# Optimization experiments

Hardware: AMD Instinct MI355X
Metric: run time of the kernel (lower is better)

## Reference

```python
import jax, jax.numpy as jnp
import numpy as np
import math

D_MODEL = 1024
NHEAD = 16
D_HEAD = D_MODEL // NHEAD
TAU = 300.0
DELTA = 5.0 * 60.0  # delta_minutes -> seconds


def setup_inputs() -> dict:
    key = jax.random.key(0)
    ks = jax.random.split(key, 10)
    B, M = 4, 2048
    H = jax.random.normal(ks[0], (B, M, D_MODEL), dtype=jnp.float32)
    patch_mask = jax.random.randint(ks[1], (B, M), 0, 2).astype(jnp.int32)
    s = 1.0 / math.sqrt(D_MODEL)
    Wq = jax.random.normal(ks[2], (D_MODEL, D_MODEL), dtype=jnp.float32) * s
    bq = jnp.zeros((D_MODEL,), dtype=jnp.float32)
    Wk = jax.random.normal(ks[3], (D_MODEL, D_MODEL), dtype=jnp.float32) * s
    bk = jnp.zeros((D_MODEL,), dtype=jnp.float32)
    Wv = jax.random.normal(ks[4], (D_MODEL, D_MODEL), dtype=jnp.float32) * s
    bv = jnp.zeros((D_MODEL,), dtype=jnp.float32)
    Wo = jax.random.normal(ks[5], (D_MODEL, D_MODEL), dtype=jnp.float32) * s
    bo = jnp.zeros((D_MODEL,), dtype=jnp.float32)
    return {"H": H, "patch_mask": patch_mask, "Wq": Wq, "bq": bq,
            "Wk": Wk, "bk": bk, "Wv": Wv, "bv": bv, "Wo": Wo, "bo": bo}


def _time_bias(M):
    idx = jnp.arange(M)
    dist = jnp.abs(idx[:, None] - idx[None, :]).astype(jnp.float32) * DELTA
    w = jnp.exp(-dist / max(TAU, 1e-6))
    return jnp.log(w + 1e-12)  # (M, M)


def reference(H, patch_mask, Wq, bq, Wk, bk, Wv, bv, Wo, bo):
    B, M, D = H.shape
    nh, dh = NHEAD, D_HEAD
    # projections -> (B, nh, M, dh)
    q = (H @ Wq.T + bq).reshape(B, M, nh, dh).transpose(0, 2, 1, 3)
    k = (H @ Wk.T + bk).reshape(B, M, nh, dh).transpose(0, 2, 1, 3)
    v = (H @ Wv.T + bv).reshape(B, M, nh, dh).transpose(0, 2, 1, 3)
    attn = jnp.einsum('bhqd,bhkd->bhqk', q, k) / math.sqrt(dh)
    attn = attn + _time_bias(M)[None, None, :, :]
    key_pad = patch_mask <= 0  # (B, M)
    attn = jnp.where(key_pad[:, None, None, :], -1e9, attn)
    A = jax.nn.softmax(attn, axis=-1)
    out = jnp.einsum('bhqk,bhkd->bhqd', A, v)
    out = out.transpose(0, 2, 1, 3).reshape(B, M, D)
    out = out @ Wo.T + bo
    out = out * patch_mask[:, :, None].astype(out.dtype)
    return out
```

## Files before the change

### kernel.cpp

```cpp
#include <hip/hip_runtime.h>
#include <stdint.h>

typedef short short8 __attribute__((ext_vector_type(8)));
typedef float f32x4 __attribute__((ext_vector_type(4)));

#define B_    4
#define M_    2048
#define D_    1024
#define NH_   16
#define DH_   64
#define LOG2E 1.44269504f

__device__ __forceinline__ short f2bf(float f) {
  union { float f; uint32_t u; } v; v.f = f;
  uint32_t r = (v.u + 0x7fffu + ((v.u >> 16) & 1u)) >> 16;
  return (short)r;
}

__device__ __forceinline__ void gl_lds16(const void* g, void* l) {
  __builtin_amdgcn_global_load_lds(
      (__attribute__((address_space(1))) void*)(g),
      (__attribute__((address_space(3))) void*)(l),
      16, 0, 0);
}

__device__ __forceinline__ f32x4 mfma16(short8 a, short8 b, f32x4 c) {
  return __builtin_amdgcn_mfma_f32_16x16x32_bf16(a, b, c, 0, 0, 0);
}

__global__ __launch_bounds__(256) void cvt_all(const float* __restrict__ H,
                                               const float* __restrict__ s0,
                                               const float* __restrict__ s1,
                                               const float* __restrict__ s2,
                                               const float* __restrict__ s3,
                                               short* __restrict__ dH,
                                               short* __restrict__ d0,
                                               short* __restrict__ d1,
                                               short* __restrict__ d2,
                                               short* __restrict__ d3) {
  const int bidx = blockIdx.x;
  const float* src;
  short* dst;
  int i;
  if (bidx < 8192) {
    src = H; dst = dH; i = bidx * 256 + threadIdx.x;
  } else {
    const int y = (bidx - 8192) >> 10;
    src = (y == 0) ? s0 : (y == 1) ? s1 : (y == 2) ? s2 : s3;
    dst = (y == 0) ? d0 : (y == 1) ? d1 : (y == 2) ? d2 : d3;
    i = ((bidx - 8192) & 1023) * 256 + threadIdx.x;
  }
  float4 v = ((const float4*)src)[i];
  short4 o;
  o.x = f2bf(v.x); o.y = f2bf(v.y); o.z = f2bf(v.z); o.w = f2bf(v.w);
  ((short4*)dst)[i] = o;
}

__global__ __launch_bounds__(256, 2) void gemm_qkv(const short* __restrict__ A,
                                                   const short* __restrict__ Wqb,
                                                   const short* __restrict__ Wkb,
                                                   const short* __restrict__ Wvb,
                                                   const float* __restrict__ bq,
                                                   const float* __restrict__ bk,
                                                   const float* __restrict__ bv,
                                                   short* __restrict__ Qo,
                                                   short* __restrict__ Ko,
                                                   short* __restrict__ Vo) {
  __shared__ char smem_raw[65536];
  short* Ab0 = (short*)smem_raw;
  short* Ab1 = (short*)(smem_raw + 8192);

  const int L = blockIdx.x + 8 * blockIdx.y;
  const int xcd = L & 7;
  const int s = L >> 3;
  const int m_local = s & 7;
  const int nt = s >> 3;
  const int m0 = (xcd * 8 + m_local) * 128;
  const int n0 = nt * 128;

  const int tid = threadIdx.x;
  const int w = tid >> 6, l = tid & 63;
  const int q4 = l >> 4, c = l & 15;
  const int wr = w >> 1, wc = w & 1;

  f32x4 acc[3][4][4] = {};
  const int arow = (l >> 2);
  const int acol = ((l & 3) ^ ((l >> 3) & 3)) * 8;
  const int q4s = (q4 ^ ((c >> 1) & 3)) * 8;

  const short* Bz0 = Wqb;
  const short* Bz1 = Wkb;
  const short* Bz2 = Wvb;

#pragma unroll
  for (int st = 0; st < 2; ++st) {
    const int chunk = w * 2 + st;
    const size_t roff = (size_t)(chunk * 16 + arow) * 1024 + acol;
    gl_lds16(A + (size_t)m0 * 1024 + roff, Ab0 + chunk * 512);
    gl_lds16(Bz0 + (size_t)n0 * 1024 + roff, (short*)(smem_raw + 16384) + chunk * 512);
    gl_lds16(Bz1 + (size_t)n0 * 1024 + roff, (short*)(smem_raw + 32768) + chunk * 512);
    gl_lds16(Bz2 + (size_t)n0 * 1024 + roff, (short*)(smem_raw + 49152) + chunk * 512);
  }
  __syncthreads();

  for (int kk = 0; kk < 32; ++kk) {
    const int cur = kk & 1;
    if (kk + 1 < 32) {
      const int k0n = (kk + 1) * 32;
#pragma unroll
      for (int st = 0; st < 2; ++st) {
        const int chunk = w * 2 + st;
        const size_t roff = (size_t)(chunk * 16 + arow) * 1024 + k0n + acol;
        gl_lds16(A + (size_t)m0 * 1024 + roff, (cur ? Ab0 : Ab1) + chunk * 512);
        gl_lds16(Bz0 + (size_t)n0 * 1024 + roff,
                 (short*)(smem_raw + 16384 + (cur ? 0 : 8192)) + chunk * 512);
        gl_lds16(Bz1 + (size_t)n0 * 1024 + roff,
                 (short*)(smem_raw + 32768 + (cur ? 0 : 8192)) + chunk * 512);
        gl_lds16(Bz2 + (size_t)n0 * 1024 + roff,
                 (short*)(smem_raw + 49152 + (cur ? 0 : 8192)) + chunk * 512);
      }
    }
    const short* Ab = cur ? Ab1 : Ab0;
    short8 af[4];
#pragma unroll
    for (int i = 0; i < 4; ++i)
      af[i] = *(const short8*)(Ab + (wr * 64 + i * 16 + c) * 32 + q4s);
#pragma unroll
    for (int z = 0; z < 3; ++z) {
      const short* Bb =
          (const short*)(smem_raw + 16384 + z * 16384 + (cur ? 8192 : 0));
      short8 bfr[4];
#pragma unroll
      for (int j = 0; j < 4; ++j)
        bfr[j] = *(const short8*)(Bb + (wc * 64 + j * 16 + c) * 32 + q4s);
#pragma unroll
      for (int i = 0; i < 4; ++i)
#pragma unroll
        for (int j = 0; j < 4; ++j)
          acc[z][i][j] = mfma16(af[i], bfr[j], acc[z][i][j]);
    }
    __syncthreads();
  }

#pragma unroll
  for (int z = 0; z < 2; ++z) {
    short* Cb = (short*)smem_raw;
    const float* bias = z ? bk : bq;
    short* outp = z ? Ko : Qo;
    const float scale = z ? 1.0f : 0.125f;
#pragma unroll
    for (int j = 0; j < 4; ++j) {
      const float bvv = bias[n0 + wc * 64 + j * 16 + c];
#pragma unroll
      for (int i = 0; i < 4; ++i)
#pragma unroll
        for (int r = 0; r < 4; ++r)
          Cb[(wr * 64 + i * 16 + q4 * 4 + r) * 136 + wc * 64 + j * 16 + c] =
              f2bf((acc[z][i][j][r] + bvv) * scale);
    }
    __syncthreads();
#pragma unroll
    for (int p = 0; p < 8; ++p) {
      const int g = p * 256 + tid;
      const int row = g >> 4, seg = g & 15;
      *(short8*)(outp + (size_t)(m0 + row) * 1024 + n0 + seg * 8) =
          *(const short8*)(Cb + row * 136 + seg * 8);
    }
    __syncthreads();
  }
  {
    short* Cb = (short*)smem_raw;
#pragma unroll
    for (int j = 0; j < 4; ++j) {
      const float bvv = bv[n0 + wc * 64 + j * 16 + c];
#pragma unroll
      for (int i = 0; i < 4; ++i) {
        short4 pk;
        pk.x = f2bf(acc[2][i][j][0] + bvv);
        pk.y = f2bf(acc[2][i][j][1] + bvv);
        pk.z = f2bf(acc[2][i][j][2] + bvv);
        pk.w = f2bf(acc[2][i][j][3] + bvv);
        *(short4*)(Cb + (wc * 64 + j * 16 + c) * 136 + wr * 64 + i * 16 + q4 * 4) = pk;
      }
    }
    __syncthreads();
    const int bb = m0 >> 11;
    const int tokb = m0 & 2047;
#pragma unroll
    for (int p = 0; p < 8; ++p) {
      const int g = p * 256 + tid;
      const int col = g >> 4, rseg = g & 15;
      const int colg = n0 + col;
      const int hh = colg >> 6, dd = colg & 63;
      *(short8*)(Vo + ((size_t)(bb * NH_ + hh) * DH_ + dd) * M_ + tokb + rseg * 8) =
          *(const short8*)(Cb + col * 136 + rseg * 8);
    }
  }
}

__global__ __launch_bounds__(256) void gemm_oproj(const short* __restrict__ A,
                                                  const short* __restrict__ Bt,
                                                  const float* __restrict__ bias,
                                                  const int* __restrict__ pmask,
                                                  float* __restrict__ outp) {
  __shared__ char smem[24576];
  short* Ab0 = (short*)smem;
  short* Ab1 = (short*)(smem + 8192);
  short* Bb0 = (short*)(smem + 16384);
  short* Bb1 = (short*)(smem + 20480);

  const int L = blockIdx.x + 16 * blockIdx.y;
  const int xcd = L & 7;
  const int s = L >> 3;
  const int m_local = s & 7;
  const int nt = s >> 3;
  const int m0 = (xcd * 8 + m_local) * 128;
  const int n0 = nt * 64;

  const int tid = threadIdx.x;
  const int w = tid >> 6, l = tid & 63;
  const int q4 = l >> 4, c = l & 15;
  const int wr = w >> 1, wc = w & 1;

  f32x4 acc[4][2] = {};
  const int arow = (l >> 2);
  const int acol = (l & 3) * 8;

#pragma unroll
  for (int st = 0; st < 2; ++st) {
    const int chunk = w * 2 + st;
    gl_lds16(A + (size_t)(m0 + chunk * 16 + arow) * 1024 + acol, Ab0 + chunk * 512);
  }
  gl_lds16(Bt + (size_t)(n0 + w * 16 + arow) * 1024 + acol, Bb0 + w * 512);
  __syncthreads();

  for (int kk = 0; kk < 32; ++kk) {
    const int cur = kk & 1;
    if (kk + 1 < 32) {
      const int k0n = (kk + 1) * 32;
#pragma unroll
      for (int st = 0; st < 2; ++st) {
        const int chunk = w * 2 + st;
        gl_lds16(A + (size_t)(m0 + chunk * 16 + arow) * 1024 + k0n + acol,
                 (cur ? Ab0 : Ab1) + chunk * 512);
      }
      gl_lds16(Bt + (size_t)(n0 + w * 16 + arow) * 1024 + k0n + acol,
               (cur ? Bb0 : Bb1) + w * 512);
    }
    const short* Ab = cur ? Ab1 : Ab0;
    const short* Bb = cur ? Bb1 : Bb0;
    short8 af[4], bfr[2];
#pragma unroll
    for (int i = 0; i < 4; ++i)
      af[i] = *(const short8*)(Ab + (wr * 64 + i * 16 + c) * 32 + q4 * 8);
#pragma unroll
    for (int j = 0; j < 2; ++j)
      bfr[j] = *(const short8*)(Bb + (wc * 32 + j * 16 + c) * 32 + q4 * 8);
#pragma unroll
    for (int i = 0; i < 4; ++i)
#pragma unroll
      for (int j = 0; j < 2; ++j)
        acc[i][j] = mfma16(af[i], bfr[j], acc[i][j]);
    __syncthreads();
  }

  float* Cf = (float*)smem;
#pragma unroll
  for (int half = 0; half < 2; ++half) {
    __syncthreads();
    if (wr == half) {
#pragma unroll
      for (int j = 0; j < 2; ++j) {
        const float bvv = bias[n0 + wc * 32 + j * 16 + c];
#pragma unroll
        for (int i = 0; i < 4; ++i)
#pragma unroll
          for (int r = 0; r < 4; ++r)
            Cf[(i * 16 + q4 * 4 + r) * 68 + wc * 32 + j * 16 + c] =
                acc[i][j][r] + bvv;
      }
    }
    __syncthreads();
#pragma unroll
    for (int p = 0; p < 4; ++p) {
      const int g = p * 256 + tid;
      const int row = g >> 4, seg = g & 15;
      const int rowg = m0 + half * 64 + row;
      const float mmv = (pmask[rowg] > 0) ? 1.0f : 0.0f;
      float4 v = *(const float4*)(Cf + row * 68 + seg * 4);
      v.x *= mmv; v.y *= mmv; v.z *= mmv; v.w *= mmv;
      *(float4*)(outp + (size_t)rowg * 1024 + n0 + seg * 4) = v;
    }
  }
}

__global__ __launch_bounds__(256) void attn_kernel(const short* __restrict__ Qb,
                                                   const short* __restrict__ Kb,
                                                   const short* __restrict__ Vtb,
                                                   const int* __restrict__ pmask,
                                                   short* __restrict__ Attb) {
  __shared__ char smem[20480];
  short* Ks0 = (short*)smem;
  short* Ks1 = (short*)(smem + 4096);
  short* Vs0 = (short*)(smem + 8192);
  short* Vs1 = (short*)(smem + 12288);
  short* Ps  = (short*)(smem + 16384);

  const int tid = threadIdx.x;
  const int w = tid >> 6, l = tid & 63;
  const int q4 = l >> 4, c = l & 15;
  const int qt = blockIdx.x, h = blockIdx.y, b = blockIdx.z;
  const short* Qrow = Qb + (size_t)(b * M_) * D_ + h * DH_;
  const short* Kbase = Kb + (size_t)(b * M_) * D_ + h * DH_;
  const short* Vbase = Vtb + (size_t)(b * NH_ + h) * DH_ * M_;
  const int qrow0 = qt * 64 + w * 16;

  short8 aq0 = *(const short8*)(Qrow + (size_t)(qrow0 + c) * D_ + q4 * 8);
  short8 aq1 = *(const short8*)(Qrow + (size_t)(qrow0 + c) * D_ + 32 + q4 * 8);

  const int jt0 = max(0, 2 * qt - 2);
  const int jt1 = min(M_ / 32 - 1, 2 * qt + 3);

  const int kh = tid >> 7, krow = (tid >> 2) & 31, ch = tid & 3;
  const int vrow = tid >> 2;

  {
    const int j0 = jt0 * 32;
    gl_lds16(Kbase + (size_t)(j0 + krow) * D_ + kh * 32 + ch * 8, (char*)Ks0 + tid * 16);
    gl_lds16(Vbase + (size_t)vrow * M_ + j0 + ch * 8, (char*)Vs0 + tid * 16);
  }
  __syncthreads();

  f32x4 o[4] = {};
  float lrun[4] = {0.f, 0.f, 0.f, 0.f};
  short* Pw = Ps + w * 512;

  for (int jt = jt0; jt <= jt1; ++jt) {
    const int buf = (jt - jt0) & 1;
    const int j0 = jt * 32;
    if (jt < jt1) {
      const int j0n = j0 + 32;
      gl_lds16(Kbase + (size_t)(j0n + krow) * D_ + kh * 32 + ch * 8,
               (char*)(buf ? Ks0 : Ks1) + tid * 16);
      gl_lds16(Vbase + (size_t)vrow * M_ + j0n + ch * 8,
               (char*)(buf ? Vs0 : Vs1) + tid * 16);
    }
    const short* Kt = buf ? Ks1 : Ks0;
    const short* Vt = buf ? Vs1 : Vs0;
    short8 b00 = *(const short8*)(Kt + c * 32 + q4 * 8);
    short8 b10 = *(const short8*)(Kt + 1024 + c * 32 + q4 * 8);
    short8 b01 = *(const short8*)(Kt + (16 + c) * 32 + q4 * 8);
    short8 b11 = *(const short8*)(Kt + 1024 + (16 + c) * 32 + q4 * 8);
    f32x4 s0 = {}, s1 = {};
    s0 = mfma16(aq0, b00, s0);
    s0 = mfma16(aq1, b10, s0);
    s1 = mfma16(aq0, b01, s1);
    s1 = mfma16(aq1, b11, s1);

    const float w0m = (pmask[b * M_ + j0 + c] > 0) ? 1.f : 0.f;
    const float w1m = (pmask[b * M_ + j0 + 16 + c] > 0) ? 1.f : 0.f;

#pragma unroll
    for (int r = 0; r < 4; ++r) {
      const int qr = qrow0 + q4 * 4 + r;
      const float d0 = fminf(fabsf((float)(qr - (j0 + c))), 28.0f);
      const float d1 = fminf(fabsf((float)(qr - (j0 + 16 + c))), 28.0f);
      const float p0 = exp2f((s0[r] - d0) * LOG2E) * w0m;
      const float p1 = exp2f((s1[r] - d1) * LOG2E) * w1m;
      Pw[(q4 * 4 + r) * 32 + c] = f2bf(p0);
      Pw[(q4 * 4 + r) * 32 + 16 + c] = f2bf(p1);
      lrun[r] += p0 + p1;
    }
    short8 pa = *(const short8*)(Pw + c * 32 + q4 * 8);
#pragma unroll
    for (int f = 0; f < 4; ++f) {
      short8 bv = *(const short8*)(Vt + (f * 16 + c) * 32 + q4 * 8);
      o[f] = mfma16(pa, bv, o[f]);
    }
    __syncthreads();
  }

#pragma unroll
  for (int r = 0; r < 4; ++r) {
#pragma unroll
    for (int off = 1; off < 16; off <<= 1)
      lrun[r] += __shfl_xor(lrun[r], off);
  }

  short* Cb = (short*)smem;
#pragma unroll
  for (int r = 0; r < 4; ++r) {
    const float inv = 1.0f / lrun[r];
#pragma unroll
    for (int f = 0; f < 4; ++f)
      Cb[(w * 16 + q4 * 4 + r) * 72 + f * 16 + c] = f2bf(o[f][r] * inv);
  }
  __syncthreads();
#pragma unroll
  for (int p = 0; p < 2; ++p) {
    const int u = p * 256 + tid;
    const int row = u >> 3, seg = u & 7;
    *(short8*)(Attb + (size_t)(b * M_ + qt * 64 + row) * D_ + h * DH_ + seg * 8) =
        *(const short8*)(Cb + row * 72 + seg * 8);
  }
}

extern "C" void kernel_launch(void* const* d_in, const int* in_sizes, int n_in,
                              void* d_out, int out_size, void* d_ws, size_t ws_size,
                              hipStream_t stream) {
  const float* H     = (const float*)d_in[0];
  const int*   pmask = (const int*)d_in[1];
  const float* Wq    = (const float*)d_in[2];
  const float* bq    = (const float*)d_in[3];
  const float* Wk    = (const float*)d_in[4];
  const float* bk    = (const float*)d_in[5];
  const float* Wv    = (const float*)d_in[6];
  const float* bv    = (const float*)d_in[7];
  const float* Wo    = (const float*)d_in[8];
  const float* bo    = (const float*)d_in[9];
  float* out = (float*)d_out;
  char* ws = (char*)d_ws;

  short* Hb   = (short*)(ws);
  short* Attb = (short*)(ws);
  short* Wqb  = (short*)(ws + (16u << 20));
  short* Wkb  = (short*)(ws + (18u << 20));
  short* Wvb  = (short*)(ws + (20u << 20));
  short* Wob  = (short*)(ws + (22u << 20));
  short* Qb   = (short*)(ws + (24u << 20));
  short* Kb2  = (short*)(ws + (40u << 20));
  short* Vtb  = (short*)(ws + (56u << 20));

  cvt_all<<<8192 + 4096, 256, 0, stream>>>(H, Wq, Wk, Wv, Wo,
                                           Hb, Wqb, Wkb, Wvb, Wob);

  gemm_qkv<<<dim3(8, 64), 256, 0, stream>>>(Hb, Wqb, Wkb, Wvb, bq, bk, bv,
                                            Qb, Kb2, Vtb);

  attn_kernel<<<dim3(M_ / 64, NH_, B_), 256, 0, stream>>>(Qb, Kb2, Vtb, pmask, Attb);

  gemm_oproj<<<dim3(16, 64), 256, 0, stream>>>(Attb, Wob, bo, pmask, out);
}
```

Before: 213.0 us.

## Single-buffer QKV GEMM staging with fine-grained per-matrix load pipelining

Replaces the double-buffered LDS scheme in the fused QKV projection GEMM with a single buffer per operand. Reloads of each of the A, Wq, Wk, Wv tiles are issued as soon as their MFMAs finish, using explicit vmcnt/lgkmcnt waits and raw barriers. MFMA sections also get raised wave priority. This cuts LDS use from 64KB to about 34KB, which could allow more resident blocks, but it adds many more barriers per k-step and leaves less prefetch distance to hide memory latency.

```diff
diff --git a/kernel.cpp b/kernel.cpp
--- a/kernel.cpp
+++ b/kernel.cpp
@@ -27,6 +27,12 @@
 __device__ __forceinline__ f32x4 mfma16(short8 a, short8 b, f32x4 c) {
   return __builtin_amdgcn_mfma_f32_16x16x32_bf16(a, b, c, 0, 0, 0);
 }
+
+#define VM_WAIT(N)  asm volatile("s_waitcnt vmcnt(" #N ")" ::: "memory")
+#define LGKM_WAIT() asm volatile("s_waitcnt lgkmcnt(0)" ::: "memory")
+#define BAR_FENCE()                    \
+  __builtin_amdgcn_s_barrier();        \
+  __builtin_amdgcn_sched_barrier(0)
 
 __global__ __launch_bounds__(256) void cvt_all(const float* __restrict__ H,
                                                const float* __restrict__ s0,
@@ -66,9 +72,11 @@
                                                    short* __restrict__ Qo,
                                                    short* __restrict__ Ko,
                                                    short* __restrict__ Vo) {
-  __shared__ char smem_raw[65536];
-  short* Ab0 = (short*)smem_raw;
-  short* Ab1 = (short*)(smem_raw + 8192);
+  __shared__ char smem_raw[34816];
+  short* As  = (short*)smem_raw;
+  short* Bs0 = (short*)(smem_raw + 8192);
+  short* Bs1 = (short*)(smem_raw + 16384);
+  short* Bs2 = (short*)(smem_raw + 24576);
 
   const int L = blockIdx.x + 8 * blockIdx.y;
   const int xcd = L & 7;
@@ -92,55 +100,89 @@
   const short* Bz1 = Wkb;
   const short* Bz2 = Wvb;
 
-#pragma unroll
-  for (int st = 0; st < 2; ++st) {
-    const int chunk = w * 2 + st;
-    const size_t roff = (size_t)(chunk * 16 + arow) * 1024 + acol;
-    gl_lds16(A + (size_t)m0 * 1024 + roff, Ab0 + chunk * 512);
-    gl_lds16(Bz0 + (size_t)n0 * 1024 + roff, (short*)(smem_raw + 16384) + chunk * 512);
-    gl_lds16(Bz1 + (size_t)n0 * 1024 + roff, (short*)(smem_raw + 32768) + chunk * 512);
-    gl_lds16(Bz2 + (size_t)n0 * 1024 + roff, (short*)(smem_raw + 49152) + chunk * 512);
-  }
+  const int ch0 = w * 2, ch1 = w * 2 + 1;
+  const size_t ro0 = (size_t)(ch0 * 16 + arow) * 1024 + acol;
+  const size_t ro1 = (size_t)(ch1 * 16 + arow) * 1024 + acol;
+  const size_t Abase = (size_t)m0 * 1024;
+  const size_t Bbase = (size_t)n0 * 1024;
+  short* dA0 = As + ch0 * 512;  short* dA1 = As + ch1 * 512;
+  short* dB00 = Bs0 + ch0 * 512; short* dB01 = Bs0 + ch1 * 512;
+  short* dB10 = Bs1 + ch0 * 512; short* dB11 = Bs1 + ch1 * 512;
+  short* dB20 = Bs2 + ch0 * 512; short* dB21 = Bs2 + ch1 * 512;
+
+  gl_lds16(A + Abase + ro0, dA0);
+  gl_lds16(A + Abase + ro1, dA1);
+  gl_lds16(Bz0 + Bbase + ro0, dB00);
+  gl_lds16(Bz0 + Bbase + ro1, dB01);
+  gl_lds16(Bz1 + Bbase + ro0, dB10);
+  gl_lds16(Bz1 + Bbase + ro1, dB11);
+  gl_lds16(Bz2 + Bbase + ro0, dB20);
+  gl_lds16(Bz2 + Bbase + ro1, dB21);
+
+  short8 af[4], bfr[4];
+
+#define READ_A()                                                        \
+  _Pragma("unroll") for (int i = 0; i < 4; ++i)                         \
+      af[i] = *(const short8*)(As + (wr * 64 + i * 16 + c) * 32 + q4s);
+#define READ_B(Bs)                                                      \
+  _Pragma("unroll") for (int j = 0; j < 4; ++j)                         \
+      bfr[j] = *(const short8*)((Bs) + (wc * 64 + j * 16 + c) * 32 + q4s);
+#define MFMA_Z(z)                                                       \
+  __builtin_amdgcn_s_setprio(1);                                        \
+  _Pragma("unroll") for (int i = 0; i < 4; ++i)                         \
+      _Pragma("unroll") for (int j = 0; j < 4; ++j)                     \
+          acc[z][i][j] = mfma16(af[i], bfr[j], acc[z][i][j]);           \
+  __builtin_amdgcn_s_setprio(0);
+
+  for (int kk = 0; kk < 31; ++kk) {
+    const size_t ko = (size_t)(kk + 1) * 32;
+    VM_WAIT(4);
+    BAR_FENCE();
+    READ_A();
+    READ_B(Bs0);
+    MFMA_Z(0);
+    LGKM_WAIT();
+    BAR_FENCE();
+    gl_lds16(A + Abase + ko + ro0, dA0);
+    gl_lds16(A + Abase + ko + ro1, dA1);
+    gl_lds16(Bz0 + Bbase + ko + ro0, dB00);
+    gl_lds16(Bz0 + Bbase + ko + ro1, dB01);
+    VM_WAIT(6);
+    BAR_FENCE();
+    READ_B(Bs1);
+    MFMA_Z(1);
+    LGKM_WAIT();
+    BAR_FENCE();
+    gl_lds16(Bz1 + Bbase + ko + ro0, dB10);
+    gl_lds16(Bz1 + Bbase + ko + ro1, dB11);
+    VM_WAIT(6);
+    BAR_FENCE();
+    READ_B(Bs2);
+    MFMA_Z(2);
+    LGKM_WAIT();
+    BAR_FENCE();
+    gl_lds16(Bz2 + Bbase + ko + ro0, dB20);
+    gl_lds16(Bz2 + Bbase + ko + ro1, dB21);
+  }
+  VM_WAIT(4);
+  BAR_FENCE();
+  READ_A();
+  READ_B(Bs0);
+  MFMA_Z(0);
+  VM_WAIT(2);
+  BAR_FENCE();
+  READ_B(Bs1);
+  MFMA_Z(1);
+  VM_WAIT(0);
+  BAR_FENCE();
+  READ_B(Bs2);
+  MFMA_Z(2);
+
+#undef READ_A
+#undef READ_B
+#undef MFMA_Z
+
   __syncthreads();
-
-  for (int kk = 0; kk < 32; ++kk) {
-    const int cur = kk & 1;
-    if (kk + 1 < 32) {
-      const int k0n = (kk + 1) * 32;
-#pragma unroll
-      for (int st = 0; st < 2; ++st) {
-        const int chunk = w * 2 + st;
-        const size_t roff = (size_t)(chunk * 16 + arow) * 1024 + k0n + acol;
-        gl_lds16(A + (size_t)m0 * 1024 + roff, (cur ? Ab0 : Ab1) + chunk * 512);
-        gl_lds16(Bz0 + (size_t)n0 * 1024 + roff,
-                 (short*)(smem_raw + 16384 + (cur ? 0 : 8192)) + chunk * 512);
-        gl_lds16(Bz1 + (size_t)n0 * 1024 + roff,
-                 (short*)(smem_raw + 32768 + (cur ? 0 : 8192)) + chunk * 512);
-        gl_lds16(Bz2 + (size_t)n0 * 1024 + roff,
-                 (short*)(smem_raw + 49152 + (cur ? 0 : 8192)) + chunk * 512);
-      }
-    }
-    const short* Ab = cur ? Ab1 : Ab0;
-    short8 af[4];
-#pragma unroll
-    for (int i = 0; i < 4; ++i)
-      af[i] = *(const short8*)(Ab + (wr * 64 + i * 16 + c) * 32 + q4s);
-#pragma unroll
-    for (int z = 0; z < 3; ++z) {
-      const short* Bb =
-          (const short*)(smem_raw + 16384 + z * 16384 + (cur ? 8192 : 0));
-      short8 bfr[4];
-#pragma unroll
-      for (int j = 0; j < 4; ++j)
-        bfr[j] = *(const short8*)(Bb + (wc * 64 + j * 16 + c) * 32 + q4s);
-#pragma unroll
-      for (int i = 0; i < 4; ++i)
-#pragma unroll
-        for (int j = 0; j < 4; ++j)
-          acc[z][i][j] = mfma16(af[i], bfr[j], acc[z][i][j]);
-    }
-    __syncthreads();
-  }
 
 #pragma unroll
   for (int z = 0; z < 2; ++z) {
```

Measured after the change: 211.6 us. No clear change (-0.7%).

## Load QKV GEMM operands directly from global memory into registers, bypassing LDS

Applied to the files above, without the earlier changes.

The QKV projection GEMM no longer stages A and weight tiles in LDS with double buffering and barriers. Each wave now loads its MFMA fragments straight from global memory into registers, software-pipelined across the Q/K/V accumulations, and raises wave priority around the MFMA groups with s_setprio. LDS shrinks to what the epilogue needs. This removes LDS traffic and per-iteration barriers, but each wave now loads its fragments separately, so data shared between waves is fetched from global or cache more than once. The final iteration also issues a wrap-around prefetch that loads data which is never used.

```diff
diff --git a/kernel.cpp b/kernel.cpp
--- a/kernel.cpp
+++ b/kernel.cpp
@@ -66,9 +66,7 @@
                                                    short* __restrict__ Qo,
                                                    short* __restrict__ Ko,
                                                    short* __restrict__ Vo) {
-  __shared__ char smem_raw[65536];
-  short* Ab0 = (short*)smem_raw;
-  short* Ab1 = (short*)(smem_raw + 8192);
+  __shared__ char smem_raw[34816];
 
   const int L = blockIdx.x + 8 * blockIdx.y;
   const int xcd = L & 7;
@@ -84,63 +82,49 @@
   const int wr = w >> 1, wc = w & 1;
 
   f32x4 acc[3][4][4] = {};
-  const int arow = (l >> 2);
-  const int acol = ((l & 3) ^ ((l >> 3) & 3)) * 8;
-  const int q4s = (q4 ^ ((c >> 1) & 3)) * 8;
-
-  const short* Bz0 = Wqb;
-  const short* Bz1 = Wkb;
-  const short* Bz2 = Wvb;
-
-#pragma unroll
-  for (int st = 0; st < 2; ++st) {
-    const int chunk = w * 2 + st;
-    const size_t roff = (size_t)(chunk * 16 + arow) * 1024 + acol;
-    gl_lds16(A + (size_t)m0 * 1024 + roff, Ab0 + chunk * 512);
-    gl_lds16(Bz0 + (size_t)n0 * 1024 + roff, (short*)(smem_raw + 16384) + chunk * 512);
-    gl_lds16(Bz1 + (size_t)n0 * 1024 + roff, (short*)(smem_raw + 32768) + chunk * 512);
-    gl_lds16(Bz2 + (size_t)n0 * 1024 + roff, (short*)(smem_raw + 49152) + chunk * 512);
-  }
-  __syncthreads();
-
-  for (int kk = 0; kk < 32; ++kk) {
-    const int cur = kk & 1;
-    if (kk + 1 < 32) {
-      const int k0n = (kk + 1) * 32;
-#pragma unroll
-      for (int st = 0; st < 2; ++st) {
-        const int chunk = w * 2 + st;
-        const size_t roff = (size_t)(chunk * 16 + arow) * 1024 + k0n + acol;
-        gl_lds16(A + (size_t)m0 * 1024 + roff, (cur ? Ab0 : Ab1) + chunk * 512);
-        gl_lds16(Bz0 + (size_t)n0 * 1024 + roff,
-                 (short*)(smem_raw + 16384 + (cur ? 0 : 8192)) + chunk * 512);
-        gl_lds16(Bz1 + (size_t)n0 * 1024 + roff,
-                 (short*)(smem_raw + 32768 + (cur ? 0 : 8192)) + chunk * 512);
-        gl_lds16(Bz2 + (size_t)n0 * 1024 + roff,
-                 (short*)(smem_raw + 49152 + (cur ? 0 : 8192)) + chunk * 512);
-      }
-    }
-    const short* Ab = cur ? Ab1 : Ab0;
-    short8 af[4];
-#pragma unroll
-    for (int i = 0; i < 4; ++i)
-      af[i] = *(const short8*)(Ab + (wr * 64 + i * 16 + c) * 32 + q4s);
-#pragma unroll
-    for (int z = 0; z < 3; ++z) {
-      const short* Bb =
-          (const short*)(smem_raw + 16384 + z * 16384 + (cur ? 8192 : 0));
-      short8 bfr[4];
-#pragma unroll
-      for (int j = 0; j < 4; ++j)
-        bfr[j] = *(const short8*)(Bb + (wc * 64 + j * 16 + c) * 32 + q4s);
-#pragma unroll
-      for (int i = 0; i < 4; ++i)
-#pragma unroll
-        for (int j = 0; j < 4; ++j)
-          acc[z][i][j] = mfma16(af[i], bfr[j], acc[z][i][j]);
-    }
-    __syncthreads();
-  }
+
+  const short* Ap = A   + (size_t)(m0 + wr * 64 + c) * 1024 + q4 * 8;
+  const short* Bq_ = Wqb + (size_t)(n0 + wc * 64 + c) * 1024 + q4 * 8;
+  const short* Bk_ = Wkb + (size_t)(n0 + wc * 64 + c) * 1024 + q4 * 8;
+  const short* Bv_ = Wvb + (size_t)(n0 + wc * 64 + c) * 1024 + q4 * 8;
+
+  short8 aE[4], aO[4], bX[4], bY[4];
+
+#define LD4(dst, base, kofs)                                              \
+  _Pragma("unroll") for (int u = 0; u < 4; ++u)                           \
+      dst[u] = *(const short8*)((base) + u * 16384 + (kofs));
+#define MM(z, a, b)                                                       \
+  __builtin_amdgcn_s_setprio(1);                                          \
+  _Pragma("unroll") for (int i = 0; i < 4; ++i)                           \
+      _Pragma("unroll") for (int j = 0; j < 4; ++j)                       \
+          acc[z][i][j] = mfma16(a[i], b[j], acc[z][i][j]);                \
+  __builtin_amdgcn_s_setprio(0);
+
+  LD4(aE, Ap, 0);
+  LD4(bX, Bq_, 0);
+
+  for (int t = 0; t < 32; t += 2) {
+    const int k0 = t * 32;
+    const int k1 = k0 + 32;
+    const int k2 = ((t + 2) & 31) * 32;
+    LD4(bY, Bk_, k0);
+    MM(0, aE, bX);
+    LD4(bX, Bv_, k0);
+    MM(1, aE, bY);
+    LD4(aO, Ap, k1);
+    LD4(bY, Bq_, k1);
+    MM(2, aE, bX);
+    LD4(bX, Bk_, k1);
+    MM(0, aO, bY);
+    LD4(bY, Bv_, k1);
+    MM(1, aO, bX);
+    LD4(aE, Ap, k2);
+    LD4(bX, Bq_, k2);
+    MM(2, aO, bY);
+  }
+
+#undef LD4
+#undef MM
 
 #pragma unroll
   for (int z = 0; z < 2; ++z) {
```

Measured after the change: 367.0 us. +72.3%, slower.
